# Optimization experiments

Measured on AMD Instinct MI355X. Metric: run time of the kernel, lower is better.

## Reference

```python
import jax, jax.numpy as jnp
import numpy as np

TOPK = 2  # from init_kwargs


def setup_inputs() -> dict:
    key = jax.random.key(0)
    ks = jax.random.split(key, 6)
    B, T, H, S, r, ad = 2, 4096, 2048, 32, 16, 32
    h = jax.random.normal(ks[0], (B, T, H), dtype=jnp.float32)
    Wr = jax.random.normal(ks[1], (S, H), dtype=jnp.float32) * 0.02
    U = jax.random.normal(ks[2], (S, H, r), dtype=jnp.float32) * 0.02
    V = jax.random.normal(ks[3], (S, r, H), dtype=jnp.float32) * 0.02
    attr = jax.random.normal(ks[4], (S, ad), dtype=jnp.float32) * 0.02
    Wa = jax.random.normal(ks[5], (1, ad), dtype=jnp.float32) * 0.02
    return {"h": h, "Wr": Wr, "U": U, "V": V, "attr": attr, "Wa": Wa}


def reference(h, Wr, U, V, attr, Wa):
    S = Wr.shape[0]
    sc = jnp.einsum('bth,sh->bts', h, Wr)                      # router logits (B,T,S)
    _, idx = jax.lax.top_k(sc, TOPK)                           # (B,T,topk)
    m = jax.nn.one_hot(idx, S, dtype=sc.dtype).sum(axis=-2)    # topk mask (B,T,S)
    g = jax.nn.softmax(sc, axis=-1) * m
    g = g / (g.sum(axis=-1, keepdims=True) + 1e-8)
    # dense all-schema low-rank transform; fuse gate+V to avoid (B,T,S,H) buffer
    hU = jnp.einsum('bth,shr->btsr', h, U)                     # (B,T,S,r)
    out = jnp.einsum('bts,btsr,srh->bth', g, hU, V)            # (B,T,H)
    aw = jax.nn.sigmoid(attr @ Wa[0])                          # (S,)
    gate = (g @ aw)[..., None]                                 # (B,T,1)
    return out * (0.9 + 0.2 * gate)
```

## Files before the change

kernel.cpp:

```cpp
#include <hip/hip_runtime.h>
#include <cstddef>

#define BT   8192
#define HD   2048
#define NS   32
#define RDIM 16
#define AD   32
#define CAP  2048


__device__ __forceinline__ float dot4(const float4 a, const float4 b) {
    return a.x * b.x + a.y * b.y + a.z * b.z + a.w * b.w;
}
__device__ __forceinline__ void fma4(float4& o, const float a, const float4 b) {
    o.x += a * b.x; o.y += a * b.y; o.z += a * b.z; o.w += a * b.w;
}

__global__ __launch_bounds__(256) void k_prep(const float* __restrict__ U,
                                              int* __restrict__ cnt,
                                              float* __restrict__ UT) {
    const int bx = blockIdx.x;
    if (bx == NS * 8) { if (threadIdx.x < 64) cnt[threadIdx.x] = 0; return; }
    const int s = bx >> 3, jc = bx & 7;
    const int j = jc * 256 + threadIdx.x;
    const float4* Up = (const float4*)(U + ((size_t)s * HD + j) * RDIM);
    const float4 a = Up[0], b = Up[1], c = Up[2], d = Up[3];
    float* Tp = UT + (size_t)s * RDIM * HD + j;
    Tp[0]       = a.x; Tp[HD]      = a.y; Tp[2*HD]   = a.z; Tp[3*HD]   = a.w;
    Tp[4*HD]    = b.x; Tp[5*HD]    = b.y; Tp[6*HD]   = b.z; Tp[7*HD]   = b.w;
    Tp[8*HD]    = c.x; Tp[9*HD]    = c.y; Tp[10*HD]  = c.z; Tp[11*HD]  = c.w;
    Tp[12*HD]   = d.x; Tp[13*HD]   = d.y; Tp[14*HD]  = d.z; Tp[15*HD]  = d.w;
}

__global__ __launch_bounds__(256) void k_router(
    const float* __restrict__ h, const float* __restrict__ Wr,
    const float* __restrict__ attr, const float* __restrict__ Wa,
    int* __restrict__ cnt, int* __restrict__ tok_list, float* __restrict__ cf_list)
{
    __shared__ float sc_s[8][NS + 1];
    const int tid = threadIdx.x, w = tid >> 6, lane = tid & 63;
    const int t0 = blockIdx.x * 8;

    #pragma unroll 1
    for (int g = 0; g < 2; ++g) {
        const int sb = w * 8 + g * 4;
        float vals[32];
        #pragma unroll
        for (int m = 0; m < 32; ++m) vals[m] = 0.f;

        float4 hA[8], hB[8];
        #pragma unroll
        for (int t = 0; t < 8; ++t)
            hA[t] = *(const float4*)(h + (size_t)(t0 + t) * HD + lane * 4);

        #pragma unroll 1
        for (int c = 0; c < 8; c += 2) {
            #pragma unroll
            for (int t = 0; t < 8; ++t)
                hB[t] = *(const float4*)(h + (size_t)(t0 + t) * HD + (c + 1) * 256 + lane * 4);
            #pragma unroll
            for (int sl = 0; sl < 4; ++sl) {
                const float4 wv = *(const float4*)(Wr + (size_t)(sb + sl) * HD + c * 256 + lane * 4);
                #pragma unroll
                for (int t = 0; t < 8; ++t) vals[t * 4 + sl] += dot4(hA[t], wv);
            }
            if (c < 6) {
                #pragma unroll
                for (int t = 0; t < 8; ++t)
                    hA[t] = *(const float4*)(h + (size_t)(t0 + t) * HD + (c + 2) * 256 + lane * 4);
            }
            #pragma unroll
            for (int sl = 0; sl < 4; ++sl) {
                const float4 wv = *(const float4*)(Wr + (size_t)(sb + sl) * HD + (c + 1) * 256 + lane * 4);
                #pragma unroll
                for (int t = 0; t < 8; ++t) vals[t * 4 + sl] += dot4(hB[t], wv);
            }
        }

        #pragma unroll
        for (int st = 0; st < 5; ++st) {
            const int d = 1 << st;
            const bool up = (lane & d) != 0;
            const int half = 16 >> st;
            #pragma unroll
            for (int i = 0; i < half; ++i) {
                const float lo = vals[2 * i], hi = vals[2 * i + 1];
                const float keep = up ? hi : lo, send = up ? lo : hi;
                vals[i] = keep + __shfl_xor(send, d, 64);
            }
        }
        vals[0] += __shfl_xor(vals[0], 32, 64);
        if (lane < 32)
            sc_s[lane >> 2][sb + (lane & 3)] = vals[0];
    }
    __syncthreads();

    if (tid < 8) {
        const int t = tid;
        float m1 = -1e30f, m2 = -1e30f;
        int i1 = 0, i2 = 0;
        #pragma unroll 1
        for (int sI = 0; sI < NS; ++sI) {
            const float v = sc_s[t][sI];
            if (v > m1) { m2 = m1; i2 = i1; m1 = v; i1 = sI; }
            else if (v > m2) { m2 = v; i2 = sI; }
        }
        float Z = 0.f;
        #pragma unroll 1
        for (int sI = 0; sI < NS; ++sI) Z += __expf(sc_s[t][sI] - m1);
        const float e2  = __expf(m2 - m1);
        const float den = 1.f + e2 + 1e-8f * Z;
        const float G1 = 1.f / den, G2 = e2 / den;
        float d1 = 0.f, d2 = 0.f;
        #pragma unroll 1
        for (int d = 0; d < AD; ++d) {
            d1 += attr[i1 * AD + d] * Wa[d];
            d2 += attr[i2 * AD + d] * Wa[d];
        }
        const float aw1 = 1.f / (1.f + __expf(-d1));
        const float aw2 = 1.f / (1.f + __expf(-d2));
        const float mult = 0.9f + 0.2f * (G1 * aw1 + G2 * aw2);
        const float c1 = G1 * mult, c2 = G2 * mult;
        const int gt = t0 + t;
        int p = atomicAdd(cnt + i1, 1);
        if (p < CAP) { tok_list[i1 * CAP + p] = gt; cf_list[i1 * CAP + p] = c1; }
        p = atomicAdd(cnt + NS + i2, 1);
        if (p < CAP) { tok_list[(NS + i2) * CAP + p] = gt; cf_list[(NS + i2) * CAP + p] = c2; }
    }
}

__global__ __launch_bounds__(256) void k_A(
    const float* __restrict__ h, const int* __restrict__ cnt,
    const int* __restrict__ tok_list, const float* __restrict__ cf_list,
    const float* __restrict__ UT, float* __restrict__ y_ws)
{
    const int g = blockIdx.x, s = g & (NS - 1);
    int count = cnt[g]; if (count > CAP) count = CAP;
    const int tid = threadIdx.x, w = tid >> 6, lane = tid & 63;
    const float* UTs = UT + (size_t)s * RDIM * HD;

    #pragma unroll 1
    for (int ci = blockIdx.y; ci * 16 < count; ci += gridDim.y) {
        int tok[4]; float cf[4];
        #pragma unroll
        for (int r = 0; r < 4; ++r) {
            const int idx = ci * 16 + w * 4 + r;
            const bool vld = idx < count;
            tok[r] = vld ? tok_list[g * CAP + idx] : 0;
            cf[r]  = vld ? cf_list[g * CAP + idx] : 0.f;
        }

        float vals[64];
        #pragma unroll
        for (int m = 0; m < 64; ++m) vals[m] = 0.f;

        float4 hA[4], hB[4];
        #pragma unroll
        for (int r = 0; r < 4; ++r)
            hA[r] = *(const float4*)(h + (size_t)tok[r] * HD + lane * 4);

        #pragma unroll 1
        for (int c = 0; c < 8; c += 2) {
            #pragma unroll
            for (int r = 0; r < 4; ++r)
                hB[r] = *(const float4*)(h + (size_t)tok[r] * HD + (c + 1) * 256 + lane * 4);
            #pragma unroll
            for (int kg = 0; kg < 4; ++kg) {
                #pragma unroll
                for (int q = 0; q < 4; ++q) {
                    const float4 uv = *(const float4*)(UTs + (size_t)(kg * 4 + q) * HD + c * 256 + lane * 4);
                    #pragma unroll
                    for (int r = 0; r < 4; ++r)
                        vals[r * 16 + kg * 4 + q] += dot4(hA[r], uv);
                }
            }
            if (c < 6) {
                #pragma unroll
                for (int r = 0; r < 4; ++r)
                    hA[r] = *(const float4*)(h + (size_t)tok[r] * HD + (c + 2) * 256 + lane * 4);
            }
            #pragma unroll
            for (int kg = 0; kg < 4; ++kg) {
                #pragma unroll
                for (int q = 0; q < 4; ++q) {
                    const float4 uv = *(const float4*)(UTs + (size_t)(kg * 4 + q) * HD + (c + 1) * 256 + lane * 4);
                    #pragma unroll
                    for (int r = 0; r < 4; ++r)
                        vals[r * 16 + kg * 4 + q] += dot4(hB[r], uv);
                }
            }
        }

        #pragma unroll
        for (int st = 0; st < 6; ++st) {
            const int d = 1 << st;
            const bool up = (lane & d) != 0;
            const int half = 32 >> st;
            #pragma unroll
            for (int i = 0; i < half; ++i) {
                const float lo = vals[2 * i], hi = vals[2 * i + 1];
                const float keep = up ? hi : lo, send = up ? lo : hi;
                vals[i] = keep + __shfl_xor(send, d, 64);
            }
        }
        const int rsel = lane >> 4;
        const float cfv = rsel == 0 ? cf[0] : rsel == 1 ? cf[1] : rsel == 2 ? cf[2] : cf[3];
        y_ws[(size_t)g * (CAP * 16) + (size_t)(ci * 16 + w * 4) * 16 + lane] = vals[0] * cfv;
    }
}

__global__ __launch_bounds__(256) void k_B(
    const float* __restrict__ V, const int* __restrict__ cnt,
    const int* __restrict__ tok_list, const float* __restrict__ y_ws,
    float* __restrict__ out, const int slot)
{
    __shared__ __align__(16) float ylds[256];
    __shared__ int toks_s[16];
    const int gsch = blockIdx.x;
    const int g = slot * NS + gsch;
    int count = cnt[g]; if (count > CAP) count = CAP;
    const int tid = threadIdx.x, w = tid >> 6, lane = tid & 63;
    const float* Vs = V + (size_t)gsch * RDIM * HD;

    #pragma unroll 1
    for (int ci = blockIdx.y; ci * 16 < count; ci += gridDim.y) {
        __syncthreads();
        if (tid < 16)
            toks_s[tid] = (ci * 16 + tid < count) ? tok_list[g * CAP + ci * 16 + tid] : -1;
        ylds[tid] = y_ws[(size_t)g * (CAP * 16) + (size_t)ci * 256 + tid];
        __syncthreads();

        int tok[4]; bool act[4];
        #pragma unroll
        for (int r = 0; r < 4; ++r) {
            const int tv = toks_s[w * 4 + r];
            act[r] = tv >= 0; tok[r] = act[r] ? tv : 0;
        }

        #pragma unroll 1
        for (int c = 0; c < 8; ++c) {
            float4 ov[4];
            if (slot) {
                #pragma unroll
                for (int r = 0; r < 4; ++r)
                    if (act[r]) ov[r] = *(const float4*)(out + (size_t)tok[r] * HD + c * 256 + lane * 4);
            }
            float4 o[4];
            #pragma unroll
            for (int r = 0; r < 4; ++r) o[r] = make_float4(0.f, 0.f, 0.f, 0.f);

            #pragma unroll
            for (int kg = 0; kg < 4; ++kg) {
                float4 vv[4];
                #pragma unroll
                for (int q = 0; q < 4; ++q)
                    vv[q] = *(const float4*)(Vs + (size_t)(kg * 4 + q) * HD + c * 256 + lane * 4);
                #pragma unroll
                for (int r = 0; r < 4; ++r) {
                    const float4 yv = *(const float4*)&ylds[(w * 4 + r) * 16 + kg * 4];
                    fma4(o[r], yv.x, vv[0]); fma4(o[r], yv.y, vv[1]);
                    fma4(o[r], yv.z, vv[2]); fma4(o[r], yv.w, vv[3]);
                }
            }
            #pragma unroll
            for (int r = 0; r < 4; ++r) {
                if (act[r]) {
                    float* op = out + (size_t)tok[r] * HD + c * 256 + lane * 4;
                    if (slot) {
                        o[r].x += ov[r].x; o[r].y += ov[r].y;
                        o[r].z += ov[r].z; o[r].w += ov[r].w;
                    }
                    *(float4*)op = o[r];
                }
            }
        }
    }
}

extern "C" void kernel_launch(void* const* d_in, const int* in_sizes, int n_in,
                              void* d_out, int out_size, void* d_ws, size_t ws_size,
                              hipStream_t stream)
{
    const float* h    = (const float*)d_in[0];
    const float* Wr   = (const float*)d_in[1];
    const float* U    = (const float*)d_in[2];
    const float* V    = (const float*)d_in[3];
    const float* attr = (const float*)d_in[4];
    const float* Wa   = (const float*)d_in[5];
    float* outp = (float*)d_out;

    char* ws = (char*)d_ws;
    int*   cnt      = (int*)ws;
    int*   tok_list = (int*)(ws + 256);
    float* cf_list  = (float*)(ws + 256 + (size_t)64 * CAP * 4);
    float* UT       = (float*)(ws + 256 + (size_t)2 * 64 * CAP * 4);
    float* y_ws     = UT + (size_t)NS * RDIM * HD;

    hipLaunchKernelGGL(k_prep,   dim3(NS * 8 + 1),  dim3(256), 0, stream, U, cnt, UT);
    hipLaunchKernelGGL(k_router, dim3(BT / 8),      dim3(256), 0, stream,
                       h, Wr, attr, Wa, cnt, tok_list, cf_list);
    hipLaunchKernelGGL(k_A,      dim3(64, 32),      dim3(256), 0, stream,
                       h, cnt, tok_list, cf_list, UT, y_ws);
    hipLaunchKernelGGL(k_B,      dim3(NS, 32),      dim3(256), 0, stream,
                       V, cnt, tok_list, y_ws, outp, 0);
    hipLaunchKernelGGL(k_B,      dim3(NS, 32),      dim3(256), 0, stream,
                       V, cnt, tok_list, y_ws, outp, 1);
}
```

Measured before the change: 274.3 us.

## Bucket tokens by expert pair and fuse down/up projections into one kernel

```diff
diff --git a/kernel.cpp b/kernel.cpp
--- a/kernel.cpp
+++ b/kernel.cpp
@@ -1,12 +1,13 @@
 #include <hip/hip_runtime.h>
 #include <cstddef>
 
-#define BT   8192
-#define HD   2048
-#define NS   32
-#define RDIM 16
-#define AD   32
-#define CAP  2048
+#define BT    8192
+#define HD    2048
+#define NS    32
+#define RDIM  16
+#define AD    32
+#define CAPP  192
+#define NPAIR (NS * NS)
 
 
 __device__ __forceinline__ float dot4(const float4 a, const float4 b) {
@@ -20,7 +21,10 @@
                                               int* __restrict__ cnt,
                                               float* __restrict__ UT) {
     const int bx = blockIdx.x;
-    if (bx == NS * 8) { if (threadIdx.x < 64) cnt[threadIdx.x] = 0; return; }
+    if (bx == NS * 8) {
+        for (int i = threadIdx.x; i < NPAIR; i += 256) cnt[i] = 0;
+        return;
+    }
     const int s = bx >> 3, jc = bx & 7;
     const int j = jc * 256 + threadIdx.x;
     const float4* Up = (const float4*)(U + ((size_t)s * HD + j) * RDIM);
@@ -35,7 +39,8 @@
 __global__ __launch_bounds__(256) void k_router(
     const float* __restrict__ h, const float* __restrict__ Wr,
     const float* __restrict__ attr, const float* __restrict__ Wa,
-    int* __restrict__ cnt, int* __restrict__ tok_list, float* __restrict__ cf_list)
+    int* __restrict__ cnt, int* __restrict__ tok_list,
+    float* __restrict__ cfa_list, float* __restrict__ cfb_list)
 {
     __shared__ float sc_s[8][NS + 1];
     const int tid = threadIdx.x, w = tid >> 6, lane = tid & 63;
@@ -122,129 +127,117 @@
         const float mult = 0.9f + 0.2f * (G1 * aw1 + G2 * aw2);
         const float c1 = G1 * mult, c2 = G2 * mult;
         const int gt = t0 + t;
-        int p = atomicAdd(cnt + i1, 1);
-        if (p < CAP) { tok_list[i1 * CAP + p] = gt; cf_list[i1 * CAP + p] = c1; }
-        p = atomicAdd(cnt + NS + i2, 1);
-        if (p < CAP) { tok_list[(NS + i2) * CAP + p] = gt; cf_list[(NS + i2) * CAP + p] = c2; }
-    }
-}
-
-__global__ __launch_bounds__(256) void k_A(
+        int lo, hi; float clo, chi;
+        if (i1 < i2) { lo = i1; hi = i2; clo = c1; chi = c2; }
+        else         { lo = i2; hi = i1; clo = c2; chi = c1; }
+        const int p = lo * NS + hi;
+        const int pos = atomicAdd(cnt + p, 1);
+        if (pos < CAPP) {
+            tok_list[p * CAPP + pos] = gt;
+            cfa_list[p * CAPP + pos] = clo;
+            cfb_list[p * CAPP + pos] = chi;
+        }
+    }
+}
+
+__device__ __forceinline__ void y_phase(const float* __restrict__ h,
+                                        const float* __restrict__ UTs,
+                                        const int (&tok)[4], const float (&cf)[4],
+                                        const int lane, float* __restrict__ yout)
+{
+    float vals[64];
+    #pragma unroll
+    for (int m = 0; m < 64; ++m) vals[m] = 0.f;
+
+    float4 hA[4], hB[4];
+    #pragma unroll
+    for (int r = 0; r < 4; ++r)
+        hA[r] = *(const float4*)(h + (size_t)tok[r] * HD + lane * 4);
+
+    #pragma unroll 1
+    for (int c = 0; c < 8; c += 2) {
+        #pragma unroll
+        for (int r = 0; r < 4; ++r)
+            hB[r] = *(const float4*)(h + (size_t)tok[r] * HD + (c + 1) * 256 + lane * 4);
+        #pragma unroll
+        for (int kg = 0; kg < 4; ++kg) {
+            #pragma unroll
+            for (int q = 0; q < 4; ++q) {
+                const float4 uv = *(const float4*)(UTs + (size_t)(kg * 4 + q) * HD + c * 256 + lane * 4);
+                #pragma unroll
+                for (int r = 0; r < 4; ++r)
+                    vals[r * 16 + kg * 4 + q] += dot4(hA[r], uv);
+            }
+        }
+        if (c < 6) {
+            #pragma unroll
+            for (int r = 0; r < 4; ++r)
+                hA[r] = *(const float4*)(h + (size_t)tok[r] * HD + (c + 2) * 256 + lane * 4);
+        }
+        #pragma unroll
+        for (int kg = 0; kg < 4; ++kg) {
+            #pragma unroll
+            for (int q = 0; q < 4; ++q) {
+                const float4 uv = *(const float4*)(UTs + (size_t)(kg * 4 + q) * HD + (c + 1) * 256 + lane * 4);
+                #pragma unroll
+                for (int r = 0; r < 4; ++r)
+                    vals[r * 16 + kg * 4 + q] += dot4(hB[r], uv);
+            }
+        }
+    }
+
+    #pragma unroll
+    for (int st = 0; st < 6; ++st) {
+        const int d = 1 << st;
+        const bool up = (lane & d) != 0;
+        const int half = 32 >> st;
+        #pragma unroll
+        for (int i = 0; i < half; ++i) {
+            const float lo = vals[2 * i], hi = vals[2 * i + 1];
+            const float keep = up ? hi : lo, send = up ? lo : hi;
+            vals[i] = keep + __shfl_xor(send, d, 64);
+        }
+    }
+    const int rsel = lane >> 4;
+    const float cfv = rsel == 0 ? cf[0] : rsel == 1 ? cf[1] : rsel == 2 ? cf[2] : cf[3];
+    yout[lane] = vals[0] * cfv;
+}
+
+__global__ __launch_bounds__(256) void k_AB(
     const float* __restrict__ h, const int* __restrict__ cnt,
-    const int* __restrict__ tok_list, const float* __restrict__ cf_list,
-    const float* __restrict__ UT, float* __restrict__ y_ws)
+    const int* __restrict__ tok_list, const float* __restrict__ cfa_list,
+    const float* __restrict__ cfb_list, const float* __restrict__ UT,
+    const float* __restrict__ V, float* __restrict__ out)
 {
-    const int g = blockIdx.x, s = g & (NS - 1);
-    int count = cnt[g]; if (count > CAP) count = CAP;
+    __shared__ __align__(16) float ya[256], yb[256];
+    const int p = blockIdx.x;
+    int count = cnt[p];
+    if (count <= 0) return;
+    if (count > CAPP) count = CAPP;
+    const int sa = p >> 5, sb = p & (NS - 1);
     const int tid = threadIdx.x, w = tid >> 6, lane = tid & 63;
-    const float* UTs = UT + (size_t)s * RDIM * HD;
+    const float* UTa = UT + (size_t)sa * RDIM * HD;
+    const float* UTb = UT + (size_t)sb * RDIM * HD;
+    const float* Va  = V  + (size_t)sa * RDIM * HD;
+    const float* Vb  = V  + (size_t)sb * RDIM * HD;
 
     #pragma unroll 1
     for (int ci = blockIdx.y; ci * 16 < count; ci += gridDim.y) {
-        int tok[4]; float cf[4];
+        int tok[4]; float cfa[4], cfb[4]; bool act[4];
         #pragma unroll
         for (int r = 0; r < 4; ++r) {
             const int idx = ci * 16 + w * 4 + r;
-            const bool vld = idx < count;
-            tok[r] = vld ? tok_list[g * CAP + idx] : 0;
-            cf[r]  = vld ? cf_list[g * CAP + idx] : 0.f;
-        }
-
-        float vals[64];
-        #pragma unroll
-        for (int m = 0; m < 64; ++m) vals[m] = 0.f;
-
-        float4 hA[4], hB[4];
-        #pragma unroll
-        for (int r = 0; r < 4; ++r)
-            hA[r] = *(const float4*)(h + (size_t)tok[r] * HD + lane * 4);
-
-        #pragma unroll 1
-        for (int c = 0; c < 8; c += 2) {
-            #pragma unroll
-            for (int r = 0; r < 4; ++r)
-                hB[r] = *(const float4*)(h + (size_t)tok[r] * HD + (c + 1) * 256 + lane * 4);
-            #pragma unroll
-            for (int kg = 0; kg < 4; ++kg) {
-                #pragma unroll
-                for (int q = 0; q < 4; ++q) {
-                    const float4 uv = *(const float4*)(UTs + (size_t)(kg * 4 + q) * HD + c * 256 + lane * 4);
-                    #pragma unroll
-                    for (int r = 0; r < 4; ++r)
-                        vals[r * 16 + kg * 4 + q] += dot4(hA[r], uv);
-                }
-            }
-            if (c < 6) {
-                #pragma unroll
-                for (int r = 0; r < 4; ++r)
-                    hA[r] = *(const float4*)(h + (size_t)tok[r] * HD + (c + 2) * 256 + lane * 4);
-            }
-            #pragma unroll
-            for (int kg = 0; kg < 4; ++kg) {
-                #pragma unroll
-                for (int q = 0; q < 4; ++q) {
-                    const float4 uv = *(const float4*)(UTs + (size_t)(kg * 4 + q) * HD + (c + 1) * 256 + lane * 4);
-                    #pragma unroll
-                    for (int r = 0; r < 4; ++r)
-                        vals[r * 16 + kg * 4 + q] += dot4(hB[r], uv);
-                }
-            }
-        }
-
-        #pragma unroll
-        for (int st = 0; st < 6; ++st) {
-            const int d = 1 << st;
-            const bool up = (lane & d) != 0;
-            const int half = 32 >> st;
-            #pragma unroll
-            for (int i = 0; i < half; ++i) {
-                const float lo = vals[2 * i], hi = vals[2 * i + 1];
-                const float keep = up ? hi : lo, send = up ? lo : hi;
-                vals[i] = keep + __shfl_xor(send, d, 64);
-            }
-        }
-        const int rsel = lane >> 4;
-        const float cfv = rsel == 0 ? cf[0] : rsel == 1 ? cf[1] : rsel == 2 ? cf[2] : cf[3];
-        y_ws[(size_t)g * (CAP * 16) + (size_t)(ci * 16 + w * 4) * 16 + lane] = vals[0] * cfv;
-    }
-}
-
-__global__ __launch_bounds__(256) void k_B(
-    const float* __restrict__ V, const int* __restrict__ cnt,
-    const int* __restrict__ tok_list, const float* __restrict__ y_ws,
-    float* __restrict__ out, const int slot)
-{
-    __shared__ __align__(16) float ylds[256];
-    __shared__ int toks_s[16];
-    const int gsch = blockIdx.x;
-    const int g = slot * NS + gsch;
-    int count = cnt[g]; if (count > CAP) count = CAP;
-    const int tid = threadIdx.x, w = tid >> 6, lane = tid & 63;
-    const float* Vs = V + (size_t)gsch * RDIM * HD;
-
-    #pragma unroll 1
-    for (int ci = blockIdx.y; ci * 16 < count; ci += gridDim.y) {
-        __syncthreads();
-        if (tid < 16)
-            toks_s[tid] = (ci * 16 + tid < count) ? tok_list[g * CAP + ci * 16 + tid] : -1;
-        ylds[tid] = y_ws[(size_t)g * (CAP * 16) + (size_t)ci * 256 + tid];
-        __syncthreads();
-
-        int tok[4]; bool act[4];
-        #pragma unroll
-        for (int r = 0; r < 4; ++r) {
-            const int tv = toks_s[w * 4 + r];
-            act[r] = tv >= 0; tok[r] = act[r] ? tv : 0;
-        }
+            act[r] = idx < count;
+            tok[r] = act[r] ? tok_list[p * CAPP + idx] : 0;
+            cfa[r] = act[r] ? cfa_list[p * CAPP + idx] : 0.f;
+            cfb[r] = act[r] ? cfb_list[p * CAPP + idx] : 0.f;
+        }
+
+        y_phase(h, UTa, tok, cfa, lane, &ya[w * 64]);
+        y_phase(h, UTb, tok, cfb, lane, &yb[w * 64]);
 
         #pragma unroll 1
         for (int c = 0; c < 8; ++c) {
-            float4 ov[4];
-            if (slot) {
-                #pragma unroll
-                for (int r = 0; r < 4; ++r)
-                    if (act[r]) ov[r] = *(const float4*)(out + (size_t)tok[r] * HD + c * 256 + lane * 4);
-            }
             float4 o[4];
             #pragma unroll
             for (int r = 0; r < 4; ++r) o[r] = make_float4(0.f, 0.f, 0.f, 0.f);
@@ -254,25 +247,31 @@
                 float4 vv[4];
                 #pragma unroll
                 for (int q = 0; q < 4; ++q)
-                    vv[q] = *(const float4*)(Vs + (size_t)(kg * 4 + q) * HD + c * 256 + lane * 4);
+                    vv[q] = *(const float4*)(Va + (size_t)(kg * 4 + q) * HD + c * 256 + lane * 4);
                 #pragma unroll
                 for (int r = 0; r < 4; ++r) {
-                    const float4 yv = *(const float4*)&ylds[(w * 4 + r) * 16 + kg * 4];
+                    const float4 yv = *(const float4*)&ya[(w * 4 + r) * 16 + kg * 4];
                     fma4(o[r], yv.x, vv[0]); fma4(o[r], yv.y, vv[1]);
                     fma4(o[r], yv.z, vv[2]); fma4(o[r], yv.w, vv[3]);
                 }
             }
             #pragma unroll
-            for (int r = 0; r < 4; ++r) {
-                if (act[r]) {
-                    float* op = out + (size_t)tok[r] * HD + c * 256 + lane * 4;
-                    if (slot) {
-                        o[r].x += ov[r].x; o[r].y += ov[r].y;
-                        o[r].z += ov[r].z; o[r].w += ov[r].w;
-                    }
-                    *(float4*)op = o[r];
+            for (int kg = 0; kg < 4; ++kg) {
+                float4 vv[4];
+                #pragma unroll
+                for (int q = 0; q < 4; ++q)
+                    vv[q] = *(const float4*)(Vb + (size_t)(kg * 4 + q) * HD + c * 256 + lane * 4);
+                #pragma unroll
+                for (int r = 0; r < 4; ++r) {
+                    const float4 yv = *(const float4*)&yb[(w * 4 + r) * 16 + kg * 4];
+                    fma4(o[r], yv.x, vv[0]); fma4(o[r], yv.y, vv[1]);
+                    fma4(o[r], yv.z, vv[2]); fma4(o[r], yv.w, vv[3]);
                 }
             }
+            #pragma unroll
+            for (int r = 0; r < 4; ++r)
+                if (act[r])
+                    *(float4*)(out + (size_t)tok[r] * HD + c * 256 + lane * 4) = o[r];
         }
     }
 }
@@ -291,18 +290,14 @@
 
     char* ws = (char*)d_ws;
     int*   cnt      = (int*)ws;
-    int*   tok_list = (int*)(ws + 256);
-    float* cf_list  = (float*)(ws + 256 + (size_t)64 * CAP * 4);
-    float* UT       = (float*)(ws + 256 + (size_t)2 * 64 * CAP * 4);
-    float* y_ws     = UT + (size_t)NS * RDIM * HD;
-
-    hipLaunchKernelGGL(k_prep,   dim3(NS * 8 + 1),  dim3(256), 0, stream, U, cnt, UT);
-    hipLaunchKernelGGL(k_router, dim3(BT / 8),      dim3(256), 0, stream,
-                       h, Wr, attr, Wa, cnt, tok_list, cf_list);
-    hipLaunchKernelGGL(k_A,      dim3(64, 32),      dim3(256), 0, stream,
-                       h, cnt, tok_list, cf_list, UT, y_ws);
-    hipLaunchKernelGGL(k_B,      dim3(NS, 32),      dim3(256), 0, stream,
-                       V, cnt, tok_list, y_ws, outp, 0);
-    hipLaunchKernelGGL(k_B,      dim3(NS, 32),      dim3(256), 0, stream,
-                       V, cnt, tok_list, y_ws, outp, 1);
-}
+    int*   tok_list = (int*)(ws + 4096);
+    float* cfa_list = (float*)(ws + 4096 + (size_t)NPAIR * CAPP * 4);
+    float* cfb_list = (float*)(ws + 4096 + (size_t)2 * NPAIR * CAPP * 4);
+    float* UT       = (float*)(ws + 4096 + (size_t)3 * NPAIR * CAPP * 4);
+
+    hipLaunchKernelGGL(k_prep,   dim3(NS * 8 + 1), dim3(256), 0, stream, U, cnt, UT);
+    hipLaunchKernelGGL(k_router, dim3(BT / 8),     dim3(256), 0, stream,
+                       h, Wr, attr, Wa, cnt, tok_list, cfa_list, cfb_list);
+    hipLaunchKernelGGL(k_AB,     dim3(NPAIR, 2),   dim3(256), 0, stream,
+                       h, cnt, tok_list, cfa_list, cfb_list, UT, V, outp);
+}
```

New measurement: 337.6 us. 1.23x slower.
